# Optimization experiments

Measured on AMD Instinct MI355X. Metric: run time of the kernel, lower is better.

The kernel has to match this reference:

```python
import jax, jax.numpy as jnp
import numpy as np

EMB = 128  # embsize
WORD = 128  # word_size
ITERS = 2


def _agg(embeds, neibors):
    # embeds: [B, N, D], neibors: [B, N, K] indices into node axis N (per batch)
    # mean-pool gathered neighbor embeddings -> [B, N, D]
    gathered = jax.vmap(lambda e, idx: e[idx])(embeds, neibors)  # [B, N, K, D]
    return gathered.mean(axis=2)


def setup_inputs() -> dict:
    key = jax.random.key(0)
    ks = jax.random.split(key, 9)
    B, N, K = 64, 512, 16
    word_embs = jax.random.normal(ks[0], (B, N, WORD), dtype=jnp.float32)
    lib_embs = jax.random.normal(ks[1], (B, N, WORD), dtype=jnp.float32)
    neibors = jax.random.randint(ks[2], (B, N, K), 0, N)
    neibors_lib = jax.random.randint(ks[3], (B, N, K), 0, N)
    mask = jax.random.uniform(ks[4], (B, N), dtype=jnp.float32)
    # xavier-uniform style params
    def xav(k, shape):
        bound = float(np.sqrt(6.0 / (shape[0] + shape[1])))
        return jax.random.uniform(k, shape, dtype=jnp.float32, minval=-bound, maxval=bound)
    weight = xav(ks[5], (WORD, EMB))
    weight2 = xav(ks[6], (EMB, EMB))
    enc_w1 = xav(ks[7], (WORD, EMB))
    enc_w2 = xav(ks[8], (EMB, EMB))
    return {"word_embs": word_embs, "neibors": neibors, "lib_embs": lib_embs,
            "neibors_lib": neibors_lib, "mask": mask, "weight": weight,
            "weight2": weight2, "enc_w1": enc_w1, "enc_w2": enc_w2}


def reference(word_embs, neibors, lib_embs, neibors_lib, mask, weight, weight2, enc_w1, enc_w2):
    B, N, _ = word_embs.shape
    # lib aggregation is loop-invariant (lib_embs fixed); same math as in-loop recompute
    agg_lib = jnp.einsum('bnw,we->bne', _agg(lib_embs, neibors_lib), weight)  # [B, N, EMB]
    word_proj = jnp.einsum('bnw,we->bne', word_embs, enc_w1)  # loop-invariant
    last_embed = jnp.zeros((B, N, EMB), dtype=jnp.float32)
    for _ in range(ITERS):
        agg_func = _agg(last_embed, neibors)  # [B, N, EMB]
        last_embed = jnp.tanh(word_proj + jnp.einsum('bne,ef->bnf', agg_func, enc_w2) + agg_lib)
    # masked sum over nodes, then final linear
    pooled = (last_embed * mask[:, :, None]).sum(axis=1)  # [B, EMB]
    return pooled @ weight2
```

## Files before the change

kernel.cpp:

```cpp
#include <hip/hip_runtime.h>
#include <hip/hip_bf16.h>

#define B_   64
#define N_   512
#define K_   16
#define D_   128
#define NPB  32
#define G1   ((B_*N_)/NPB)

typedef float f32x4  __attribute__((ext_vector_type(4)));
typedef short bf16x8 __attribute__((ext_vector_type(8)));

static __device__ __forceinline__ short f2bf(float x) {
    union { float f; unsigned u; } v; v.f = x;
    unsigned r = v.u + 0x7fffu + ((v.u >> 16) & 1u);
    return (short)(r >> 16);
}
static __device__ __forceinline__ float bfbits2f(unsigned hi_bits) {
    return __uint_as_float(hi_bits);
}
static __device__ __forceinline__ float fast_tanh(float x) {
    float e = __expf(2.f * x);
    return 1.f - 2.f * __builtin_amdgcn_rcpf(e + 1.f);
}

__global__ __launch_bounds__(256) void pack_kernel(const float* __restrict__ enc1,
                                                   const float* __restrict__ wgt,
                                                   const float* __restrict__ enc2,
                                                   short* __restrict__ Bp1,
                                                   short* __restrict__ Bp2) {
    int tid = blockIdx.x * 256 + threadIdx.x;
    short out[8];
    if (tid < 4096) {
        int l = tid & 63, nt = (tid >> 6) & 7, ks = tid >> 9;
        int k0 = ks * 32 + (l >> 4) * 8;
        int col = nt * 16 + (l & 15);
#pragma unroll
        for (int j = 0; j < 8; ++j) {
            int r = k0 + j;
            float v = (r < 128) ? enc1[r * 128 + col] : wgt[(r - 128) * 128 + col];
            out[j] = f2bf(v);
        }
        *(int4*)&Bp1[(size_t)tid * 8] = *(int4*)out;
    } else if (tid < 6144) {
        int t2 = tid - 4096;
        int l = t2 & 63, nt = (t2 >> 6) & 7, ks = t2 >> 9;
        int k0 = ks * 32 + (l >> 4) * 8;
        int col = nt * 16 + (l & 15);
#pragma unroll
        for (int j = 0; j < 8; ++j) out[j] = f2bf(enc2[(k0 + j) * 128 + col]);
        *(int4*)&Bp2[(size_t)t2 * 8] = *(int4*)out;
    }
}

static __device__ __forceinline__ int swz_blk() {
    const int hw = blockIdx.x;
    return ((hw & 7) << 7) + (hw >> 3);
}

#define LDA1 264
__global__ __launch_bounds__(256) void gemm1(const float* __restrict__ word,
                                             const int* __restrict__ nbrL,
                                             const float* __restrict__ lib,
                                             const short* __restrict__ Bp1,
                                             float* __restrict__ base,
                                             short* __restrict__ t1) {
    __shared__ short sA[NPB * LDA1];
    __shared__ int sIdx[NPB * 16];
    const int tid = threadIdx.x;
    const int blk = swz_blk();
    const int b = blk >> 4;
    const int node0 = blk * NPB;

    if (tid < 128) *(int4*)&sIdx[tid * 4] = *(const int4*)&nbrL[(size_t)node0 * 16 + tid * 4];
    __syncthreads();

    const int w = tid >> 6, l = tid & 63;
    const int rh = l >> 5, c4 = l & 31;
    const float* libB = lib + (size_t)b * N_ * D_;

#pragma unroll 2
    for (int p = 0; p < 4; ++p) {
        const int row = 8 * w + 2 * p + rh;
        const int gid = node0 + row;
        float4 wv = *(const float4*)&word[(size_t)gid * D_ + c4 * 4];
        short4 ws; ws.x = f2bf(wv.x); ws.y = f2bf(wv.y); ws.z = f2bf(wv.z); ws.w = f2bf(wv.w);
        *(short4*)&sA[row * LDA1 + c4 * 4] = ws;
        int idxr[16];
#pragma unroll
        for (int k = 0; k < 16; ++k) idxr[k] = sIdx[row * 16 + k];
        float4 s = {0.f, 0.f, 0.f, 0.f};
#pragma unroll
        for (int k = 0; k < 16; ++k) {
            float4 lv = *(const float4*)&libB[(size_t)idxr[k] * D_ + c4 * 4];
            s.x += lv.x; s.y += lv.y; s.z += lv.z; s.w += lv.w;
        }
        short4 as; as.x = f2bf(s.x * 0.0625f); as.y = f2bf(s.y * 0.0625f);
        as.z = f2bf(s.z * 0.0625f); as.w = f2bf(s.w * 0.0625f);
        *(short4*)&sA[row * LDA1 + 128 + c4 * 4] = as;
    }
    __syncthreads();

    const int rt = w & 1, nh = w >> 1;
    f32x4 acc[4];
#pragma unroll
    for (int j = 0; j < 4; ++j) acc[j] = (f32x4)0.f;

    const int arow = rt * 16 + (l & 15);
#pragma unroll
    for (int ks = 0; ks < 8; ++ks) {
        bf16x8 a = *(const bf16x8*)&sA[arow * LDA1 + ks * 32 + (l >> 4) * 8];
#pragma unroll
        for (int j = 0; j < 4; ++j) {
            const int nt = nh * 4 + j;
            bf16x8 bb = *(const bf16x8*)&Bp1[((size_t)(ks * 8 + nt) * 64 + l) * 8];
            acc[j] = __builtin_amdgcn_mfma_f32_16x16x32_bf16(a, bb, acc[j], 0, 0, 0);
        }
    }

    const int r0 = rt * 16 + (l >> 4) * 4;
    const int cl = l & 15;
#pragma unroll
    for (int j = 0; j < 4; ++j) {
        const int col = (nh * 4 + j) * 16 + cl;
#pragma unroll
        for (int r = 0; r < 4; ++r) {
            size_t o = (size_t)(node0 + r0 + r) * D_ + col;
            float v = acc[j][r];
            base[o] = v;
            t1[o] = f2bf(fast_tanh(v));
        }
    }
}

#define LDA2 136
__global__ __launch_bounds__(256) void gemm2(const short* __restrict__ t1,
                                             const int* __restrict__ nbr,
                                             const short* __restrict__ Bp2,
                                             const float* __restrict__ base,
                                             const float* __restrict__ mask,
                                             const float* __restrict__ w2,
                                             float* __restrict__ out) {
    __shared__ short sA[NPB * LDA2];
    __shared__ int sIdx[NPB * 16];
    __shared__ float pred[2][128];
    __shared__ float tot[128];
    const int tid = threadIdx.x;
    const int blk = swz_blk();
    const int b = blk >> 4;
    const int node0 = blk * NPB;

    if (tid < 128) *(int4*)&sIdx[tid * 4] = *(const int4*)&nbr[(size_t)node0 * 16 + tid * 4];
    __syncthreads();

    const int w = tid >> 6, l = tid & 63;
    const int rh = l >> 5, c4 = l & 31;
    const short* t1B = t1 + (size_t)b * N_ * D_;

#pragma unroll 2
    for (int p = 0; p < 4; ++p) {
        const int row = 8 * w + 2 * p + rh;
        int idxr[16];
#pragma unroll
        for (int k = 0; k < 16; ++k) idxr[k] = sIdx[row * 16 + k];
        float s0 = 0.f, s1 = 0.f, s2 = 0.f, s3 = 0.f;
#pragma unroll
        for (int k = 0; k < 16; ++k) {
            uint2 u = *(const uint2*)&t1B[(size_t)idxr[k] * D_ + c4 * 4];
            s0 += bfbits2f(u.x << 16); s1 += bfbits2f(u.x & 0xffff0000u);
            s2 += bfbits2f(u.y << 16); s3 += bfbits2f(u.y & 0xffff0000u);
        }
        short4 as; as.x = f2bf(s0 * 0.0625f); as.y = f2bf(s1 * 0.0625f);
        as.z = f2bf(s2 * 0.0625f); as.w = f2bf(s3 * 0.0625f);
        *(short4*)&sA[row * LDA2 + c4 * 4] = as;
    }
    __syncthreads();

    const int rt = w & 1, nh = w >> 1;
    f32x4 acc[4];
#pragma unroll
    for (int j = 0; j < 4; ++j) acc[j] = (f32x4)0.f;

    const int arow = rt * 16 + (l & 15);
#pragma unroll
    for (int ks = 0; ks < 4; ++ks) {
        bf16x8 a = *(const bf16x8*)&sA[arow * LDA2 + ks * 32 + (l >> 4) * 8];
#pragma unroll
        for (int j = 0; j < 4; ++j) {
            const int nt = nh * 4 + j;
            bf16x8 bb = *(const bf16x8*)&Bp2[((size_t)(ks * 8 + nt) * 64 + l) * 8];
            acc[j] = __builtin_amdgcn_mfma_f32_16x16x32_bf16(a, bb, acc[j], 0, 0, 0);
        }
    }

    const int r0 = rt * 16 + (l >> 4) * 4;
    const int cl = l & 15;
#pragma unroll
    for (int j = 0; j < 4; ++j) {
        const int col = (nh * 4 + j) * 16 + cl;
        float s = 0.f;
#pragma unroll
        for (int r = 0; r < 4; ++r) {
            size_t o = (size_t)(node0 + r0 + r) * D_ + col;
            float v = fast_tanh(base[o] + acc[j][r]);
            s += v * mask[node0 + r0 + r];
        }
        s += __shfl_xor(s, 16);
        s += __shfl_xor(s, 32);
        if (l < 16) pred[rt][col] = s;
    }
    __syncthreads();
    if (tid < 128) tot[tid] = pred[0][tid] + pred[1][tid];
    __syncthreads();
    if (tid < 128) {
        float a2 = 0.f;
#pragma unroll 4
        for (int f = 0; f < 128; ++f) a2 += tot[f] * w2[f * 128 + tid];
        atomicAdd(&out[b * 128 + tid], a2);
    }
}

extern "C" void kernel_launch(void* const* d_in, const int* in_sizes, int n_in,
                              void* d_out, int out_size, void* d_ws, size_t ws_size,
                              hipStream_t stream) {
    const float* word_embs   = (const float*)d_in[0];
    const int*   neibors     = (const int*)d_in[1];
    const float* lib_embs    = (const float*)d_in[2];
    const int*   neibors_lib = (const int*)d_in[3];
    const float* mask        = (const float*)d_in[4];
    const float* weight      = (const float*)d_in[5];
    const float* weight2     = (const float*)d_in[6];
    const float* enc_w1      = (const float*)d_in[7];
    const float* enc_w2      = (const float*)d_in[8];
    float* out = (float*)d_out;

    char* ws = (char*)d_ws;
    float* base = (float*)(ws);
    short* t1   = (short*)(ws + (1u << 24));
    short* Bp1  = (short*)(ws + (1u << 24) + (1u << 23));
    short* Bp2  = (short*)(ws + (1u << 24) + (1u << 23) + 65536);

    hipMemsetAsync(out, 0, B_ * D_ * sizeof(float), stream);
    pack_kernel<<<24, 256, 0, stream>>>(enc_w1, weight, enc_w2, Bp1, Bp2);

    gemm1<<<G1, 256, 0, stream>>>(word_embs, neibors_lib, lib_embs, Bp1, base, t1);
    gemm2<<<G1, 256, 0, stream>>>(t1, neibors, Bp2, base, mask, weight2, out);
}
```

Measured before the change: 51.98 us.

## Halve nodes per block and fold output zeroing into pack kernel

```diff
diff --git a/kernel.cpp b/kernel.cpp
--- a/kernel.cpp
+++ b/kernel.cpp
@@ -5,7 +5,7 @@
 #define N_   512
 #define K_   16
 #define D_   128
-#define NPB  32
+#define NPB  16
 #define G1   ((B_*N_)/NPB)
 
 typedef float f32x4  __attribute__((ext_vector_type(4)));
@@ -28,9 +28,11 @@
                                                    const float* __restrict__ wgt,
                                                    const float* __restrict__ enc2,
                                                    short* __restrict__ Bp1,
-                                                   short* __restrict__ Bp2) {
+                                                   short* __restrict__ Bp2,
+                                                   float* __restrict__ out) {
     int tid = blockIdx.x * 256 + threadIdx.x;
-    short out[8];
+    if (tid < 8192) out[tid] = 0.f;
+    short o8[8];
     if (tid < 4096) {
         int l = tid & 63, nt = (tid >> 6) & 7, ks = tid >> 9;
         int k0 = ks * 32 + (l >> 4) * 8;
@@ -39,23 +41,23 @@
         for (int j = 0; j < 8; ++j) {
             int r = k0 + j;
             float v = (r < 128) ? enc1[r * 128 + col] : wgt[(r - 128) * 128 + col];
-            out[j] = f2bf(v);
-        }
-        *(int4*)&Bp1[(size_t)tid * 8] = *(int4*)out;
+            o8[j] = f2bf(v);
+        }
+        *(int4*)&Bp1[(size_t)tid * 8] = *(int4*)o8;
     } else if (tid < 6144) {
         int t2 = tid - 4096;
         int l = t2 & 63, nt = (t2 >> 6) & 7, ks = t2 >> 9;
         int k0 = ks * 32 + (l >> 4) * 8;
         int col = nt * 16 + (l & 15);
 #pragma unroll
-        for (int j = 0; j < 8; ++j) out[j] = f2bf(enc2[(k0 + j) * 128 + col]);
-        *(int4*)&Bp2[(size_t)t2 * 8] = *(int4*)out;
+        for (int j = 0; j < 8; ++j) o8[j] = f2bf(enc2[(k0 + j) * 128 + col]);
+        *(int4*)&Bp2[(size_t)t2 * 8] = *(int4*)o8;
     }
 }
 
 static __device__ __forceinline__ int swz_blk() {
     const int hw = blockIdx.x;
-    return ((hw & 7) << 7) + (hw >> 3);
+    return ((hw & 7) << 8) + (hw >> 3);
 }
 
 #define LDA1 264
@@ -69,19 +71,19 @@
     __shared__ int sIdx[NPB * 16];
     const int tid = threadIdx.x;
     const int blk = swz_blk();
-    const int b = blk >> 4;
+    const int b = blk >> 5;
     const int node0 = blk * NPB;
 
-    if (tid < 128) *(int4*)&sIdx[tid * 4] = *(const int4*)&nbrL[(size_t)node0 * 16 + tid * 4];
+    if (tid < 64) *(int4*)&sIdx[tid * 4] = *(const int4*)&nbrL[(size_t)node0 * 16 + tid * 4];
     __syncthreads();
 
     const int w = tid >> 6, l = tid & 63;
     const int rh = l >> 5, c4 = l & 31;
     const float* libB = lib + (size_t)b * N_ * D_;
 
-#pragma unroll 2
-    for (int p = 0; p < 4; ++p) {
-        const int row = 8 * w + 2 * p + rh;
+#pragma unroll
+    for (int p = 0; p < 2; ++p) {
+        const int row = 4 * w + 2 * p + rh;
         const int gid = node0 + row;
         float4 wv = *(const float4*)&word[(size_t)gid * D_ + c4 * 4];
         short4 ws; ws.x = f2bf(wv.x); ws.y = f2bf(wv.y); ws.z = f2bf(wv.z); ws.w = f2bf(wv.w);
@@ -101,28 +103,26 @@
     }
     __syncthreads();
 
-    const int rt = w & 1, nh = w >> 1;
-    f32x4 acc[4];
-#pragma unroll
-    for (int j = 0; j < 4; ++j) acc[j] = (f32x4)0.f;
-
-    const int arow = rt * 16 + (l & 15);
+    f32x4 acc[2];
+    acc[0] = (f32x4)0.f; acc[1] = (f32x4)0.f;
+
+    const int arow = l & 15;
 #pragma unroll
     for (int ks = 0; ks < 8; ++ks) {
         bf16x8 a = *(const bf16x8*)&sA[arow * LDA1 + ks * 32 + (l >> 4) * 8];
 #pragma unroll
-        for (int j = 0; j < 4; ++j) {
-            const int nt = nh * 4 + j;
+        for (int j = 0; j < 2; ++j) {
+            const int nt = 2 * w + j;
             bf16x8 bb = *(const bf16x8*)&Bp1[((size_t)(ks * 8 + nt) * 64 + l) * 8];
             acc[j] = __builtin_amdgcn_mfma_f32_16x16x32_bf16(a, bb, acc[j], 0, 0, 0);
         }
     }
 
-    const int r0 = rt * 16 + (l >> 4) * 4;
+    const int r0 = (l >> 4) * 4;
     const int cl = l & 15;
 #pragma unroll
-    for (int j = 0; j < 4; ++j) {
-        const int col = (nh * 4 + j) * 16 + cl;
+    for (int j = 0; j < 2; ++j) {
+        const int col = (2 * w + j) * 16 + cl;
 #pragma unroll
         for (int r = 0; r < 4; ++r) {
             size_t o = (size_t)(node0 + r0 + r) * D_ + col;
@@ -143,23 +143,22 @@
                                              float* __restrict__ out) {
     __shared__ short sA[NPB * LDA2];
     __shared__ int sIdx[NPB * 16];
-    __shared__ float pred[2][128];
-    __shared__ float tot[128];
+    __shared__ float pred[128];
     const int tid = threadIdx.x;
     const int blk = swz_blk();
-    const int b = blk >> 4;
+    const int b = blk >> 5;
     const int node0 = blk * NPB;
 
-    if (tid < 128) *(int4*)&sIdx[tid * 4] = *(const int4*)&nbr[(size_t)node0 * 16 + tid * 4];
+    if (tid < 64) *(int4*)&sIdx[tid * 4] = *(const int4*)&nbr[(size_t)node0 * 16 + tid * 4];
     __syncthreads();
 
     const int w = tid >> 6, l = tid & 63;
     const int rh = l >> 5, c4 = l & 31;
     const short* t1B = t1 + (size_t)b * N_ * D_;
 
-#pragma unroll 2
-    for (int p = 0; p < 4; ++p) {
-        const int row = 8 * w + 2 * p + rh;
+#pragma unroll
+    for (int p = 0; p < 2; ++p) {
+        const int row = 4 * w + 2 * p + rh;
         int idxr[16];
 #pragma unroll
         for (int k = 0; k < 16; ++k) idxr[k] = sIdx[row * 16 + k];
@@ -176,28 +175,26 @@
     }
     __syncthreads();
 
-    const int rt = w & 1, nh = w >> 1;
-    f32x4 acc[4];
-#pragma unroll
-    for (int j = 0; j < 4; ++j) acc[j] = (f32x4)0.f;
-
-    const int arow = rt * 16 + (l & 15);
+    f32x4 acc[2];
+    acc[0] = (f32x4)0.f; acc[1] = (f32x4)0.f;
+
+    const int arow = l & 15;
 #pragma unroll
     for (int ks = 0; ks < 4; ++ks) {
         bf16x8 a = *(const bf16x8*)&sA[arow * LDA2 + ks * 32 + (l >> 4) * 8];
 #pragma unroll
-        for (int j = 0; j < 4; ++j) {
-            const int nt = nh * 4 + j;
+        for (int j = 0; j < 2; ++j) {
+            const int nt = 2 * w + j;
             bf16x8 bb = *(const bf16x8*)&Bp2[((size_t)(ks * 8 + nt) * 64 + l) * 8];
             acc[j] = __builtin_amdgcn_mfma_f32_16x16x32_bf16(a, bb, acc[j], 0, 0, 0);
         }
     }
 
-    const int r0 = rt * 16 + (l >> 4) * 4;
+    const int r0 = (l >> 4) * 4;
     const int cl = l & 15;
 #pragma unroll
-    for (int j = 0; j < 4; ++j) {
-        const int col = (nh * 4 + j) * 16 + cl;
+    for (int j = 0; j < 2; ++j) {
+        const int col = (2 * w + j) * 16 + cl;
         float s = 0.f;
 #pragma unroll
         for (int r = 0; r < 4; ++r) {
@@ -207,15 +204,13 @@
         }
         s += __shfl_xor(s, 16);
         s += __shfl_xor(s, 32);
-        if (l < 16) pred[rt][col] = s;
-    }
-    __syncthreads();
-    if (tid < 128) tot[tid] = pred[0][tid] + pred[1][tid];
+        if (l < 16) pred[col] = s;
+    }
     __syncthreads();
     if (tid < 128) {
         float a2 = 0.f;
 #pragma unroll 4
-        for (int f = 0; f < 128; ++f) a2 += tot[f] * w2[f * 128 + tid];
+        for (int f = 0; f < 128; ++f) a2 += pred[f] * w2[f * 128 + tid];
         atomicAdd(&out[b * 128 + tid], a2);
     }
 }
@@ -240,9 +235,7 @@
     short* Bp1  = (short*)(ws + (1u << 24) + (1u << 23));
     short* Bp2  = (short*)(ws + (1u << 24) + (1u << 23) + 65536);
 
-    hipMemsetAsync(out, 0, B_ * D_ * sizeof(float), stream);
-    pack_kernel<<<24, 256, 0, stream>>>(enc_w1, weight, enc_w2, Bp1, Bp2);
-
+    pack_kernel<<<32, 256, 0, stream>>>(enc_w1, weight, enc_w2, Bp1, Bp2, out);
     gemm1<<<G1, 256, 0, stream>>>(word_embs, neibors_lib, lib_embs, Bp1, base, t1);
     gemm2<<<G1, 256, 0, stream>>>(t1, neibors, Bp2, base, mask, weight2, out);
 }
```

After: 51.28 us. About the same (-1.3%).
